# Kernel tuning notes

Hardware: AMD Instinct MI355X
Metric: run time of the kernel (lower is better)

The kernel has to match this reference:

```python
import jax, jax.numpy as jnp
import numpy as np

# 3x3 laplacian stencil, OIHW
LAP = jnp.array([-1, -1, -1, -1, 8, -1, -1, -1, -1], dtype=jnp.float32).reshape(1, 1, 3, 3)
THR = 0.1
SMOOTH = 1.0


def _lap_conv(x, stride):
    # x: [B,1,H,W]
    return jax.lax.conv_general_dilated(
        x, LAP, window_strides=(stride, stride), padding=((1, 1), (1, 1)),
        dimension_numbers=('NCHW', 'OIHW', 'NCHW'))


def _nearest_up(x, H, W):
    # PyTorch 'nearest': src_idx = floor(dst_idx * in/out)
    h, w = x.shape[2], x.shape[3]
    ri = (jnp.arange(H) * h) // H
    ci = (jnp.arange(W) * w) // W
    return x[:, :, ri][:, :, :, ci]


def _thresh(x):
    return jnp.where(x > THR, 1.0, 0.0).astype(x.dtype)


def setup_inputs() -> dict:
    key = jax.random.key(0)
    k1, k2 = jax.random.split(key)
    B, H, W = 16, 1024, 1024
    boundary_logits = jax.random.normal(k1, (B, 1, H, W), dtype=jnp.float32)
    gtmasks = (jax.random.uniform(k2, (B, H, W)) > 0.5).astype(jnp.float32)
    fuse_kernel = jnp.array([0.6, 0.3, 0.1], dtype=jnp.float32).reshape(1, 3, 1, 1)
    return {"boundary_logits": boundary_logits, "gtmasks": gtmasks, "fuse_kernel": fuse_kernel}


def reference(boundary_logits, gtmasks, fuse_kernel):
    g = gtmasks[:, None, :, :].astype(jnp.float32)  # [B,1,H,W]
    bt = _thresh(jnp.maximum(_lap_conv(g, 1), 0.0))  # full res
    H, W = bt.shape[2], bt.shape[3]
    bt2 = _thresh(_nearest_up(jnp.maximum(_lap_conv(g, 2), 0.0), H, W))
    bt4 = _thresh(_nearest_up(jnp.maximum(_lap_conv(g, 4), 0.0), H, W))
    # (x8 branch in original is computed but unused in the output)
    pyr = jnp.concatenate([bt, bt2, bt4], axis=1)  # [B,3,H,W]
    fused = jnp.einsum('bchw,c->bhw', pyr, fuse_kernel.reshape(3))[:, None]  # 1x1 fuse conv
    target = _thresh(fused)  # [B,1,H,W]

    x = boundary_logits
    # stable BCE with logits, mean reduction
    bce_loss = jnp.mean(jnp.maximum(x, 0.0) - x * target + jnp.log1p(jnp.exp(-jnp.abs(x))))

    p = jax.nn.sigmoid(x)
    n = p.shape[0]
    pf = p.reshape(n, -1)
    tf = target.reshape(n, -1)
    inter = jnp.sum(pf * tf, axis=1)
    dice_loss = jnp.mean(1.0 - (2.0 * inter + SMOOTH) / (jnp.sum(pf, 1) + jnp.sum(tf, 1) + SMOOTH))
    return bce_loss, dice_loss
```

## Files before the change

### kernel.cpp

```cpp
#include <hip/hip_runtime.h>

#define IMG_H 1024
#define IMG_W 1024
#define NIMG  16
#define NPIX  16777216.0f
#define QPI   256
#define NBLK  4096
#define LOG2E 1.44269504088896340736f
#define LN2   0.69314718055994530942f


__global__ __launch_bounds__(256) void dal_main(
    const float* __restrict__ xlogits,
    const float* __restrict__ gmask,
    const float* __restrict__ fuse,
    float* __restrict__ ws)
{
    const int bid  = blockIdx.x;
    const int img  = bid >> 8;
    const int q    = bid & 255;
    const int r0   = q << 2;
    const int tid  = (int)threadIdx.x;
    const int lane = tid & 63;
    const int j0   = tid * 4;

    const float w0 = fuse[0], w1 = fuse[1], w2 = fuse[2];

    const size_t ibase = (size_t)img * (IMG_H * IMG_W);
    const float* gi = gmask + ibase;
    const float* xi = xlogits + ibase;

    const int  jl   = (j0 > 0) ? (j0 - 1) : 0;
    const int  jr   = (j0 + 4 < IMG_W) ? (j0 + 4) : (IMG_W - 1);
    const bool hasL = (j0 > 0);
    const bool hasR = (j0 + 4 < IMG_W);

    const float* xrow = xi + (size_t)r0 * IMG_W + j0;
    float4 xv0 = *reinterpret_cast<const float4*>(xrow);
    float4 xv1 = *reinterpret_cast<const float4*>(xrow + IMG_W);
    float4 xv2 = *reinterpret_cast<const float4*>(xrow + 2 * IMG_W);
    float4 xv3 = *reinterpret_cast<const float4*>(xrow + 3 * IMG_W);

    float rm[6][4];
    float cv[4][4];
    #pragma unroll
    for (int t = 0; t < 6; ++t) {
        const int r = r0 - 1 + t;
        float vx = 0.f, vy = 0.f, vz = 0.f, vw = 0.f, lf = 0.f, rg = 0.f;
        if (r >= 0 && r < IMG_H) {
            const float* row = gi + (size_t)r * IMG_W;
            float4 v = *reinterpret_cast<const float4*>(row + j0);
            float l = row[jl];
            float g = row[jr];
            vx = v.x; vy = v.y; vz = v.z; vw = v.w;
            lf = hasL ? l : 0.f;
            rg = hasR ? g : 0.f;
        }
        rm[t][0] = fminf(lf, fminf(vx, vy));
        rm[t][1] = fminf(vx, fminf(vy, vz));
        rm[t][2] = fminf(vy, fminf(vz, vw));
        rm[t][3] = fminf(vz, fminf(vw, rg));
        if (t >= 1 && t <= 4) {
            cv[t - 1][0] = vx; cv[t - 1][1] = vy;
            cv[t - 1][2] = vz; cv[t - 1][3] = vw;
        }
    }

    float bt[4][4];
    #pragma unroll
    for (int r = 0; r < 4; ++r)
        #pragma unroll
        for (int k = 0; k < 4; ++k) {
            float cm = fminf(rm[r][k], fminf(rm[r + 1][k], rm[r + 2][k]));
            bt[r][k] = (cv[r][k] > 0.5f && cm < 0.5f) ? 1.f : 0.f;
        }

    const float wb4 = w2 * bt[0][0];
    float base2[2][2];
    base2[0][0] = fmaf(w1, bt[0][0], wb4);
    base2[0][1] = fmaf(w1, bt[0][2], wb4);
    base2[1][0] = fmaf(w1, bt[2][0], wb4);
    base2[1][1] = fmaf(w1, bt[2][2], wb4);

    float l2 = 0.f, xt = 0.f, inter = 0.f, sump = 0.f;
    int   st = 0;

    auto px = [&](float x, float btv, float b2v) {
        float f = fmaf(w0, btv, b2v);
        bool  c = f > 0.1f;
        st += (int)__popcll(__ballot(c));
        float u   = __builtin_amdgcn_exp2f(x * LOG2E);
        float opu = 1.f + u;
        float p   = u * __builtin_amdgcn_rcpf(opu);
        l2   += __builtin_amdgcn_logf(opu);
        sump += p;
        xt   += c ? x : 0.f;
        inter+= c ? p : 0.f;
    };

    px(xv0.x, bt[0][0], base2[0][0]); px(xv0.y, bt[0][1], base2[0][0]);
    px(xv0.z, bt[0][2], base2[0][1]); px(xv0.w, bt[0][3], base2[0][1]);
    px(xv1.x, bt[1][0], base2[0][0]); px(xv1.y, bt[1][1], base2[0][0]);
    px(xv1.z, bt[1][2], base2[0][1]); px(xv1.w, bt[1][3], base2[0][1]);
    px(xv2.x, bt[2][0], base2[1][0]); px(xv2.y, bt[2][1], base2[1][0]);
    px(xv2.z, bt[2][2], base2[1][1]); px(xv2.w, bt[2][3], base2[1][1]);
    px(xv3.x, bt[3][0], base2[1][0]); px(xv3.y, bt[3][1], base2[1][0]);
    px(xv3.z, bt[3][2], base2[1][1]); px(xv3.w, bt[3][3], base2[1][1]);

    float bce = fmaf(LN2, l2, -xt);

    #pragma unroll
    for (int off = 32; off > 0; off >>= 1) {
        bce   += __shfl_down(bce, off);
        inter += __shfl_down(inter, off);
        sump  += __shfl_down(sump, off);
    }
    __shared__ float red[4][4];
    const int wid = tid >> 6;
    if (lane == 0) {
        red[0][wid] = bce; red[1][wid] = inter;
        red[2][wid] = sump; red[3][wid] = (float)st;
    }
    __syncthreads();
    if (tid == 0) {
        ws[bid]            = red[0][0] + red[0][1] + red[0][2] + red[0][3];
        ws[NBLK + bid]     = red[1][0] + red[1][1] + red[1][2] + red[1][3];
        ws[2 * NBLK + bid] = red[2][0] + red[2][1] + red[2][2] + red[2][3];
        ws[3 * NBLK + bid] = red[3][0] + red[3][1] + red[3][2] + red[3][3];
    }
}

__global__ __launch_bounds__(1024) void dal_finalize(
    const float* __restrict__ ws, float* __restrict__ out)
{
    const int t    = (int)threadIdx.x;
    const int wv   = t >> 6;
    const int lane = t & 63;
    const int i0   = t * 4;

    float4 a0 = *reinterpret_cast<const float4*>(ws + i0);
    float4 a1 = *reinterpret_cast<const float4*>(ws + NBLK + i0);
    float4 a2 = *reinterpret_cast<const float4*>(ws + 2 * NBLK + i0);
    float4 a3 = *reinterpret_cast<const float4*>(ws + 3 * NBLK + i0);

    float bce   = (a0.x + a0.y) + (a0.z + a0.w);
    float inter = (a1.x + a1.y) + (a1.z + a1.w);
    float sump  = (a2.x + a2.y) + (a2.z + a2.w);
    float sumt  = (a3.x + a3.y) + (a3.z + a3.w);

    #pragma unroll
    for (int off = 32; off > 0; off >>= 1) {
        bce   += __shfl_down(bce, off);
        inter += __shfl_down(inter, off);
        sump  += __shfl_down(sump, off);
        sumt  += __shfl_down(sumt, off);
    }

    __shared__ float sb[16], sd[16];
    if (lane == 0) {
        sb[wv] = bce;
        sd[wv] = 1.f - (2.f * inter + 1.f) / (sump + sumt + 1.f);
    }
    __syncthreads();
    if (t == 0) {
        float tb = 0.f, td = 0.f;
        #pragma unroll
        for (int i = 0; i < NIMG; ++i) { tb += sb[i]; td += sd[i]; }
        out[0] = tb / NPIX;
        out[1] = td / (float)NIMG;
    }
}

extern "C" void kernel_launch(void* const* d_in, const int* in_sizes, int n_in,
                              void* d_out, int out_size, void* d_ws, size_t ws_size,
                              hipStream_t stream)
{
    const float* x    = (const float*)d_in[0];
    const float* g    = (const float*)d_in[1];
    const float* fuse = (const float*)d_in[2];
    float* out = (float*)d_out;
    float* ws  = (float*)d_ws;

    dal_main<<<NBLK, 256, 0, stream>>>(x, g, fuse, ws);
    dal_finalize<<<1, 1024, 0, stream>>>(ws, out);
}
```

Baseline: 33.27 us.

## Process eight rows per block to cut stencil halo overhead and block count

Each block now handles 8 rows instead of 4, halving the grid to 2048 blocks. The gmask halo rows drop from 6 loads per 4 rows to 10 per 8, and the two scalar edge loads per row are replaced by two overlapping float4 loads. Partial sums go into two interleaved accumulators, and per-block results are written as one float4 into an array-of-structs workspace. The cost is more registers per thread and fewer blocks to hide memory latency.

Result: faster. 31.12 us (-6.4%).

```diff
diff --git a/kernel.cpp b/kernel.cpp
--- a/kernel.cpp
+++ b/kernel.cpp
@@ -4,8 +4,8 @@
 #define IMG_W 1024
 #define NIMG  16
 #define NPIX  16777216.0f
-#define QPI   256
-#define NBLK  4096
+#define SPI   128
+#define NBLK  2048
 #define LOG2E 1.44269504088896340736f
 #define LN2   0.69314718055994530942f
 
@@ -14,12 +14,12 @@
     const float* __restrict__ xlogits,
     const float* __restrict__ gmask,
     const float* __restrict__ fuse,
-    float* __restrict__ ws)
+    float4* __restrict__ ws4)
 {
     const int bid  = blockIdx.x;
-    const int img  = bid >> 8;
-    const int q    = bid & 255;
-    const int r0   = q << 2;
+    const int img  = bid >> 7;
+    const int q    = bid & 127;
+    const int r0   = q << 3;
     const int tid  = (int)threadIdx.x;
     const int lane = tid & 63;
     const int j0   = tid * 4;
@@ -31,83 +31,90 @@
     const float* xi = xlogits + ibase;
 
     const int  jl   = (j0 > 0) ? (j0 - 1) : 0;
-    const int  jr   = (j0 + 4 < IMG_W) ? (j0 + 4) : (IMG_W - 1);
+    const int  jr1  = (j0 + 4 < IMG_W) ? (j0 + 1) : (IMG_W - 4);
     const bool hasL = (j0 > 0);
     const bool hasR = (j0 + 4 < IMG_W);
 
-    const float* xrow = xi + (size_t)r0 * IMG_W + j0;
-    float4 xv0 = *reinterpret_cast<const float4*>(xrow);
-    float4 xv1 = *reinterpret_cast<const float4*>(xrow + IMG_W);
-    float4 xv2 = *reinterpret_cast<const float4*>(xrow + 2 * IMG_W);
-    float4 xv3 = *reinterpret_cast<const float4*>(xrow + 3 * IMG_W);
-
-    float rm[6][4];
-    float cv[4][4];
+    float rm[10][4];
+    float cv[8][4];
     #pragma unroll
-    for (int t = 0; t < 6; ++t) {
+    for (int t = 0; t < 10; ++t) {
         const int r = r0 - 1 + t;
-        float vx = 0.f, vy = 0.f, vz = 0.f, vw = 0.f, lf = 0.f, rg = 0.f;
+        float c0 = 0.f, c1 = 0.f, c2 = 0.f, c3 = 0.f, c4 = 0.f, c5 = 0.f;
         if (r >= 0 && r < IMG_H) {
             const float* row = gi + (size_t)r * IMG_W;
-            float4 v = *reinterpret_cast<const float4*>(row + j0);
-            float l = row[jl];
-            float g = row[jr];
-            vx = v.x; vy = v.y; vz = v.z; vw = v.w;
-            lf = hasL ? l : 0.f;
-            rg = hasR ? g : 0.f;
+            float4 a = *reinterpret_cast<const float4*>(row + jl);
+            float4 b = *reinterpret_cast<const float4*>(row + jr1);
+            c0 = hasL ? a.x : 0.f;
+            c1 = hasL ? a.y : a.x;
+            c2 = hasL ? a.z : a.y;
+            c3 = hasL ? a.w : a.z;
+            c4 = hasR ? b.z : b.w;
+            c5 = hasR ? b.w : 0.f;
         }
-        rm[t][0] = fminf(lf, fminf(vx, vy));
-        rm[t][1] = fminf(vx, fminf(vy, vz));
-        rm[t][2] = fminf(vy, fminf(vz, vw));
-        rm[t][3] = fminf(vz, fminf(vw, rg));
-        if (t >= 1 && t <= 4) {
-            cv[t - 1][0] = vx; cv[t - 1][1] = vy;
-            cv[t - 1][2] = vz; cv[t - 1][3] = vw;
+        rm[t][0] = fminf(c0, fminf(c1, c2));
+        rm[t][1] = fminf(c1, fminf(c2, c3));
+        rm[t][2] = fminf(c2, fminf(c3, c4));
+        rm[t][3] = fminf(c3, fminf(c4, c5));
+        if (t >= 1 && t <= 8) {
+            cv[t - 1][0] = c1; cv[t - 1][1] = c2;
+            cv[t - 1][2] = c3; cv[t - 1][3] = c4;
         }
     }
 
-    float bt[4][4];
+    float bt[8][4];
     #pragma unroll
-    for (int r = 0; r < 4; ++r)
+    for (int r = 0; r < 8; ++r)
         #pragma unroll
         for (int k = 0; k < 4; ++k) {
             float cm = fminf(rm[r][k], fminf(rm[r + 1][k], rm[r + 2][k]));
             bt[r][k] = (cv[r][k] > 0.5f && cm < 0.5f) ? 1.f : 0.f;
         }
 
-    const float wb4 = w2 * bt[0][0];
-    float base2[2][2];
-    base2[0][0] = fmaf(w1, bt[0][0], wb4);
-    base2[0][1] = fmaf(w1, bt[0][2], wb4);
-    base2[1][0] = fmaf(w1, bt[2][0], wb4);
-    base2[1][1] = fmaf(w1, bt[2][2], wb4);
+    const float wb4A = w2 * bt[0][0];
+    const float wb4B = w2 * bt[4][0];
+    float base2[4][2];
+    #pragma unroll
+    for (int rp = 0; rp < 4; ++rp) {
+        const float wb = (rp < 2) ? wb4A : wb4B;
+        base2[rp][0] = fmaf(w1, bt[2 * rp][0], wb);
+        base2[rp][1] = fmaf(w1, bt[2 * rp][2], wb);
+    }
 
-    float l2 = 0.f, xt = 0.f, inter = 0.f, sump = 0.f;
-    int   st = 0;
+    float l2[2]  = {0.f, 0.f}, xt[2] = {0.f, 0.f};
+    float itr[2] = {0.f, 0.f}, sp[2] = {0.f, 0.f};
+    int st = 0;
 
-    auto px = [&](float x, float btv, float b2v) {
+    auto px = [&](float x, float btv, float b2v, int a) {
         float f = fmaf(w0, btv, b2v);
         bool  c = f > 0.1f;
         st += (int)__popcll(__ballot(c));
         float u   = __builtin_amdgcn_exp2f(x * LOG2E);
         float opu = 1.f + u;
         float p   = u * __builtin_amdgcn_rcpf(opu);
-        l2   += __builtin_amdgcn_logf(opu);
-        sump += p;
-        xt   += c ? x : 0.f;
-        inter+= c ? p : 0.f;
+        l2[a]  += __builtin_amdgcn_logf(opu);
+        sp[a]  += p;
+        xt[a]  += c ? x : 0.f;
+        itr[a] += c ? p : 0.f;
     };
 
-    px(xv0.x, bt[0][0], base2[0][0]); px(xv0.y, bt[0][1], base2[0][0]);
-    px(xv0.z, bt[0][2], base2[0][1]); px(xv0.w, bt[0][3], base2[0][1]);
-    px(xv1.x, bt[1][0], base2[0][0]); px(xv1.y, bt[1][1], base2[0][0]);
-    px(xv1.z, bt[1][2], base2[0][1]); px(xv1.w, bt[1][3], base2[0][1]);
-    px(xv2.x, bt[2][0], base2[1][0]); px(xv2.y, bt[2][1], base2[1][0]);
-    px(xv2.z, bt[2][2], base2[1][1]); px(xv2.w, bt[2][3], base2[1][1]);
-    px(xv3.x, bt[3][0], base2[1][0]); px(xv3.y, bt[3][1], base2[1][0]);
-    px(xv3.z, bt[3][2], base2[1][1]); px(xv3.w, bt[3][3], base2[1][1]);
+    const float* xrow = xi + (size_t)r0 * IMG_W + j0;
+    #pragma unroll
+    for (int r = 0; r < 8; ++r) {
+        float4 xv = *reinterpret_cast<const float4*>(xrow + (size_t)r * IMG_W);
+        const int   rp = r >> 1;
+        const int   a  = r & 1;
+        const float bA = base2[rp][0];
+        const float bB = base2[rp][1];
+        px(xv.x, bt[r][0], bA, a);
+        px(xv.y, bt[r][1], bA, a);
+        px(xv.z, bt[r][2], bB, a);
+        px(xv.w, bt[r][3], bB, a);
+    }
 
-    float bce = fmaf(LN2, l2, -xt);
+    float bce   = fmaf(LN2, l2[0] + l2[1], -(xt[0] + xt[1]));
+    float inter = itr[0] + itr[1];
+    float sump  = sp[0] + sp[1];
 
     #pragma unroll
     for (int off = 32; off > 0; off >>= 1) {
@@ -123,30 +130,28 @@
     }
     __syncthreads();
     if (tid == 0) {
-        ws[bid]            = red[0][0] + red[0][1] + red[0][2] + red[0][3];
-        ws[NBLK + bid]     = red[1][0] + red[1][1] + red[1][2] + red[1][3];
-        ws[2 * NBLK + bid] = red[2][0] + red[2][1] + red[2][2] + red[2][3];
-        ws[3 * NBLK + bid] = red[3][0] + red[3][1] + red[3][2] + red[3][3];
+        float4 o;
+        o.x = red[0][0] + red[0][1] + red[0][2] + red[0][3];
+        o.y = red[1][0] + red[1][1] + red[1][2] + red[1][3];
+        o.z = red[2][0] + red[2][1] + red[2][2] + red[2][3];
+        o.w = red[3][0] + red[3][1] + red[3][2] + red[3][3];
+        ws4[bid] = o;
     }
 }
 
 __global__ __launch_bounds__(1024) void dal_finalize(
-    const float* __restrict__ ws, float* __restrict__ out)
+    const float4* __restrict__ ws4, float* __restrict__ out)
 {
     const int t    = (int)threadIdx.x;
     const int wv   = t >> 6;
     const int lane = t & 63;
-    const int i0   = t * 4;
 
-    float4 a0 = *reinterpret_cast<const float4*>(ws + i0);
-    float4 a1 = *reinterpret_cast<const float4*>(ws + NBLK + i0);
-    float4 a2 = *reinterpret_cast<const float4*>(ws + 2 * NBLK + i0);
-    float4 a3 = *reinterpret_cast<const float4*>(ws + 3 * NBLK + i0);
-
-    float bce   = (a0.x + a0.y) + (a0.z + a0.w);
-    float inter = (a1.x + a1.y) + (a1.z + a1.w);
-    float sump  = (a2.x + a2.y) + (a2.z + a2.w);
-    float sumt  = (a3.x + a3.y) + (a3.z + a3.w);
+    float4 a = ws4[2 * t];
+    float4 b = ws4[2 * t + 1];
+    float bce   = a.x + b.x;
+    float inter = a.y + b.y;
+    float sump  = a.z + b.z;
+    float sumt  = a.w + b.w;
 
     #pragma unroll
     for (int off = 32; off > 0; off >>= 1) {
@@ -179,8 +184,8 @@
     const float* g    = (const float*)d_in[1];
     const float* fuse = (const float*)d_in[2];
     float* out = (float*)d_out;
-    float* ws  = (float*)d_ws;
+    float4* ws4 = (float4*)d_ws;
 
-    dal_main<<<NBLK, 256, 0, stream>>>(x, g, fuse, ws);
-    dal_finalize<<<1, 1024, 0, stream>>>(ws, out);
+    dal_main<<<NBLK, 256, 0, stream>>>(x, g, fuse, ws4);
+    dal_finalize<<<1, 1024, 0, stream>>>(ws4, out);
 }
```
